# Performance work log

Hardware: AMD Instinct MI355X
Metric: run time of the kernel (lower is better)

The kernel has to match this reference:

```python
import jax, jax.numpy as jnp
import numpy as np

B, T, D_IN, D_H, D_CODE, N_CODES, D_OUT = 64, 512, 1024, 512, 256, 128, 100


def setup_inputs() -> dict:
    key = jax.random.key(0)
    ks = jax.random.split(key, 8)
    x = jax.random.normal(ks[0], (B, T, D_IN), dtype=jnp.float32)
    W1 = jax.random.normal(ks[1], (D_IN, D_H), dtype=jnp.float32) * (1.0 / np.sqrt(D_IN))
    b1 = jnp.zeros((D_H,), jnp.float32)
    W2 = jax.random.normal(ks[2], (D_H, D_CODE), dtype=jnp.float32) * (1.0 / np.sqrt(D_H))
    b2 = jnp.zeros((D_CODE,), jnp.float32)
    codebook = jax.random.normal(ks[3], (N_CODES, D_CODE), dtype=jnp.float32)
    Wd = jax.random.normal(ks[4], (D_CODE, D_OUT), dtype=jnp.float32) * (1.0 / np.sqrt(D_CODE))
    bd = jnp.zeros((D_OUT,), jnp.float32)
    return {"x": x, "W1": W1, "b1": b1, "W2": W2, "b2": b2,
            "codebook": codebook, "Wd": Wd, "bd": bd}


def reference(x, W1, b1, W2, b2, codebook, Wd, bd):
    Bb, Tt, _ = x.shape
    # Encoder (per-timestep loop in torch == one batched matmul)
    h = jax.nn.relu(jnp.einsum('btd,dh->bth', x, W1) + b1)
    encoded = jnp.einsum('bth,hc->btc', h, W2) + b2          # [B,T,256]
    flat = encoded.reshape(-1, D_CODE)                        # [B*T,256]
    # Squared euclidean distances (argmin identical to cdist argmin)
    d2 = (jnp.sum(flat * flat, axis=1, keepdims=True)
          - 2.0 * flat @ codebook.T
          + jnp.sum(codebook * codebook, axis=1))             # [B*T,128]
    token_indices = jnp.argmin(d2, axis=-1)                   # [B*T]
    quantized = codebook[token_indices].reshape(Bb, Tt, D_CODE)
    commitment_loss = jnp.mean((encoded - jax.lax.stop_gradient(quantized)) ** 2)
    codebook_loss = jnp.mean((quantized - jax.lax.stop_gradient(encoded)) ** 2)
    # decoded is computed in the torch model but never returned (dead code)
    pooled = encoded.mean(axis=1)
    decoded = pooled @ Wd + bd  # noqa: F841 (pruned by XLA, kept for fidelity)
    total_loss = commitment_loss + 0.25 * codebook_loss
    return (token_indices.reshape(Bb, Tt), commitment_loss, codebook_loss, total_loss)
```

## Files before the change

### kernel.cpp

```cpp
#include <hip/hip_runtime.h>
#include <cstddef>
#include <cstdint>

static constexpr int M_ROWS  = 32768;
static constexpr int D_INK   = 1024;
static constexpr int D_HID   = 512;
static constexpr int D_CODE_ = 256;
static constexpr int N_CODES_= 128;

static constexpr float TAU_GAP = 0.15f;

using f16x8 = __attribute__((ext_vector_type(8))) _Float16;
using f32x4 = __attribute__((ext_vector_type(4))) float;
using f32x2 = __attribute__((ext_vector_type(2))) float;

__device__ __forceinline__ float rdlane(float v, int kk) {
    return __uint_as_float(__builtin_amdgcn_readlane(__float_as_uint(v), kk));
}


__device__ __forceinline__ void dma16(const void* g, void* l) {
    __builtin_amdgcn_global_load_lds(
        (const __attribute__((address_space(1))) void*)g,
        (__attribute__((address_space(3))) void*)l, 16, 0, 0);
}

__device__ __forceinline__ void stage_panel(const _Float16* __restrict__ p,
                                            _Float16* dst, int w, int lane)
{
    #pragma unroll
    for (int ii = 0; ii < 2; ++ii) {
        const int I = 2 * w + ii;
        dma16(p + (size_t)I * 512 + lane * 8, dst + (size_t)I * 512);
    }
}

__device__ __forceinline__ void mfma_tile(const _Float16* sA, const _Float16* sB,
                                          int wm, int wn, int kq, int lm,
                                          f32x4 (&acc)[4][4])
{
    f16x8 a[4];
    #pragma unroll
    for (int fm = 0; fm < 4; ++fm)
        a[fm] = *(const f16x8*)(sA + (kq * 128 + wm * 64 + fm * 16 + lm) * 8);
    #pragma unroll
    for (int fn = 0; fn < 4; ++fn) {
        const f16x8 b = *(const f16x8*)(sB + (kq * 128 + wn * 64 + fn * 16 + lm) * 8);
        #pragma unroll
        for (int fm = 0; fm < 4; ++fm)
            acc[fm][fn] = __builtin_amdgcn_mfma_f32_16x16x32_f16(a[fm], b, acc[fm][fn], 0, 0, 0);
    }
}

__device__ __forceinline__ int xcd_swz(int bid, int nwg) {
    const int q = nwg >> 3;
    return (bid & 7) * q + (bid >> 3);
}

__global__ __launch_bounds__(256)
void prep_cb_kernel(const float* __restrict__ cb, _Float16* __restrict__ cbP,
                    float* __restrict__ cbT,
                    float* __restrict__ cbnorm, float* __restrict__ accum,
                    int* __restrict__ cnt)
{
    const int j = blockIdx.x;
    const int t = threadIdx.x;
    const float v = cb[j * D_CODE_ + t];
    const int ks = t >> 5, kq = (t >> 3) & 3, jj = t & 7;
    cbP[((size_t)ks * 512 + kq * 128 + j) * 8 + jj] = (_Float16)v;
    cbT[(size_t)t * N_CODES_ + j] = v;

    __shared__ float sr[256];
    sr[t] = v * v;
    __syncthreads();
    for (int s = 128; s >= 1; s >>= 1) {
        if (t < s) sr[t] += sr[t + s];
        __syncthreads();
    }
    if (t == 0) cbnorm[j] = sr[0];
    if (j == 0 && t < 2) accum[t] = 0.0f;
    if (j == 0 && t == 2) *cnt = 0;
}

__global__ __launch_bounds__(256)
void pack_w_kernel(const float* __restrict__ W, _Float16* __restrict__ WP,
                   int Kd, int Nd)
{
    const int ks = blockIdx.x, nt = blockIdx.y;
    const int t = threadIdx.x;
    _Float16* dst = WP + ((size_t)nt * (Kd >> 5) + ks) * 4096;
    #pragma unroll
    for (int half = 0; half < 2; ++half) {
        const int f = half * 256 + t;
        const int nc = f & 127, kq = f >> 7;
        f16x8 v;
        #pragma unroll
        for (int j = 0; j < 8; ++j)
            v[j] = (_Float16)W[(size_t)(ks * 32 + kq * 8 + j) * Nd + nt * 128 + nc];
        *(f16x8*)(dst + (size_t)f * 8) = v;
    }
}

__global__ __launch_bounds__(256)
void pack_x_kernel(const float* __restrict__ X, _Float16* __restrict__ XP)
{
    __shared__ _Float16 sh[128][136];
    const int t  = threadIdx.x;
    const int mt = blockIdx.x;
    const int kc = blockIdx.y;

    const float* src = X + (size_t)mt * 128 * D_INK + kc * 128;
    #pragma unroll
    for (int i = 0; i < 16; ++i) {
        const int idx = i * 256 + t;
        const int row = idx >> 5, c4 = idx & 31;
        const float4 v = *(const float4*)(src + (size_t)row * D_INK + c4 * 4);
        _Float16* d = &sh[row][c4 * 4];
        d[0] = (_Float16)v.x; d[1] = (_Float16)v.y;
        d[2] = (_Float16)v.z; d[3] = (_Float16)v.w;
    }
    __syncthreads();

    _Float16* dst = XP + ((size_t)mt * 32 + kc * 4) * 4096;
    #pragma unroll
    for (int s = 0; s < 4; ++s) {
        #pragma unroll
        for (int half = 0; half < 2; ++half) {
            const int f = half * 256 + t;
            const int rc = f & 127, kq = f >> 7;
            const f16x8 v = *(const f16x8*)(&sh[rc][s * 32 + kq * 8]);
            *(f16x8*)(dst + (size_t)s * 4096 + (size_t)f * 8) = v;
        }
    }
}

__global__ __launch_bounds__(256, 4)
void gemm1_kernel(const _Float16* __restrict__ AP, const _Float16* __restrict__ BP,
                  const float* __restrict__ bias, _Float16* __restrict__ CP)
{
    __shared__ _Float16 lds[2][2][4096];

    const int tid  = threadIdx.x;
    const int lane = tid & 63;
    const int w    = tid >> 6;
    const int wm = w >> 1, wn = w & 1;
    const int kq = lane >> 4, lm = lane & 15;

    const int swz = xcd_swz(blockIdx.x, (M_ROWS / 128) * (D_HID / 128));
    const int n0 = (swz & 3) * 128;
    const int m0 = (swz >> 2) * 128;

    const _Float16* Apan = AP + ((size_t)(m0 >> 7) * 32) * 4096;
    const _Float16* Bpan = BP + ((size_t)(n0 >> 7) * 32) * 4096;

    f32x4 acc[4][4] = {};

    stage_panel(Apan, &lds[0][0][0], w, lane);
    stage_panel(Bpan, &lds[0][1][0], w, lane);

    constexpr int NSTEP = D_INK / 32;
    for (int t = 0; t < NSTEP; ++t) {
        const int cur = t & 1, nxt = cur ^ 1;
        __syncthreads();
        if (t + 1 < NSTEP) {
            stage_panel(Apan + (size_t)(t + 1) * 4096, &lds[nxt][0][0], w, lane);
            stage_panel(Bpan + (size_t)(t + 1) * 4096, &lds[nxt][1][0], w, lane);
        }
        mfma_tile(&lds[cur][0][0], &lds[cur][1][0], wm, wn, kq, lm, acc);
    }

    #pragma unroll
    for (int fn = 0; fn < 4; ++fn) {
        const int col = n0 + wn * 64 + fn * 16 + lm;
        const float bv = bias[col];
        #pragma unroll
        for (int fm = 0; fm < 4; ++fm) {
            #pragma unroll
            for (int r = 0; r < 4; ++r) {
                const int row = m0 + wm * 64 + fm * 16 + kq * 4 + r;
                const float v = fmaxf(acc[fm][fn][r] + bv, 0.0f);
                CP[(((size_t)(row >> 7) * 16 + (col >> 5)) * 512
                    + (size_t)((col >> 3) & 3) * 128 + (row & 127)) * 8 + (col & 7)]
                    = (_Float16)v;
            }
        }
    }
}

__global__ __launch_bounds__(256, 4)
void gemm2_kernel(const _Float16* __restrict__ AP, const _Float16* __restrict__ BP,
                  const float* __restrict__ bias, _Float16* __restrict__ CP,
                  float* __restrict__ accum)
{
    __shared__ _Float16 lds[2][2][4096];

    const int tid  = threadIdx.x;
    const int lane = tid & 63;
    const int w    = tid >> 6;
    const int wm = w >> 1, wn = w & 1;
    const int kq = lane >> 4, lm = lane & 15;

    const int swz = xcd_swz(blockIdx.x, (M_ROWS / 128) * (D_CODE_ / 128));
    const int n0 = (swz & 1) * 128;
    const int m0 = (swz >> 1) * 128;

    const _Float16* Apan = AP + ((size_t)(m0 >> 7) * 16) * 4096;
    const _Float16* Bpan = BP + ((size_t)(n0 >> 7) * 16) * 4096;

    f32x4 acc[4][4] = {};

    stage_panel(Apan, &lds[0][0][0], w, lane);
    stage_panel(Bpan, &lds[0][1][0], w, lane);

    constexpr int NSTEP = D_HID / 32;
    for (int t = 0; t < NSTEP; ++t) {
        const int cur = t & 1, nxt = cur ^ 1;
        __syncthreads();
        if (t + 1 < NSTEP) {
            stage_panel(Apan + (size_t)(t + 1) * 4096, &lds[nxt][0][0], w, lane);
            stage_panel(Bpan + (size_t)(t + 1) * 4096, &lds[nxt][1][0], w, lane);
        }
        mfma_tile(&lds[cur][0][0], &lds[cur][1][0], wm, wn, kq, lm, acc);
    }

    float sumsq = 0.0f;
    #pragma unroll
    for (int fn = 0; fn < 4; ++fn) {
        const int col = n0 + wn * 64 + fn * 16 + lm;
        const float bv = bias[col];
        #pragma unroll
        for (int fm = 0; fm < 4; ++fm) {
            #pragma unroll
            for (int r = 0; r < 4; ++r) {
                const int row = m0 + wm * 64 + fm * 16 + kq * 4 + r;
                const float v = acc[fm][fn][r] + bv;
                sumsq = fmaf(v, v, sumsq);
                CP[(((size_t)(row >> 7) * 8 + (col >> 5)) * 512
                    + (size_t)((col >> 3) & 3) * 128 + (row & 127)) * 8 + (col & 7)]
                    = (_Float16)v;
            }
        }
    }
    #pragma unroll
    for (int mk = 1; mk <= 32; mk <<= 1) sumsq += __shfl_xor(sumsq, mk);
    if (lane == 0) atomicAdd(&accum[1], sumsq);
}

__global__ __launch_bounds__(256, 4)
void dist_kernel(const _Float16* __restrict__ AP, const _Float16* __restrict__ BP,
                 const float* __restrict__ cbn,
                 float* __restrict__ outIdx, float* __restrict__ accum,
                 int* __restrict__ cnt, int* __restrict__ list)
{
    __shared__ _Float16 lds[2][2][4096];

    const int tid  = threadIdx.x;
    const int lane = tid & 63;
    const int w    = tid >> 6;
    const int wm = w >> 1, wn = w & 1;
    const int kq = lane >> 4, lm = lane & 15;
    const int m0 = blockIdx.x * 128;

    float cbn_l[4];
    #pragma unroll
    for (int fn = 0; fn < 4; ++fn) cbn_l[fn] = cbn[wn * 64 + fn * 16 + lm];

    const _Float16* Apan = AP + ((size_t)(m0 >> 7) * 8) * 4096;

    f32x4 acc[4][4] = {};

    stage_panel(Apan, &lds[0][0][0], w, lane);
    stage_panel(BP,   &lds[0][1][0], w, lane);

    constexpr int NSTEP = D_CODE_ / 32;
    for (int t = 0; t < NSTEP; ++t) {
        const int cur = t & 1, nxt = cur ^ 1;
        __syncthreads();
        if (t + 1 < NSTEP) {
            stage_panel(Apan + (size_t)(t + 1) * 4096, &lds[nxt][0][0], w, lane);
            stage_panel(BP   + (size_t)(t + 1) * 4096, &lds[nxt][1][0], w, lane);
        }
        mfma_tile(&lds[cur][0][0], &lds[cur][1][0], wm, wn, kq, lm, acc);
    }

    __syncthreads();
    float* eb1 = (float*)&lds[0][0][0];
    float* eb2 = eb1 + 256;
    int*   eix = (int*)(eb2 + 256);

    #pragma unroll
    for (int fm = 0; fm < 4; ++fm) {
        #pragma unroll
        for (int r = 0; r < 4; ++r) {
            float b1v = 3.4e38f, b2v = 3.4e38f; int bi = 0;
            #pragma unroll
            for (int fn = 0; fn < 4; ++fn) {
                const float v = fmaf(-2.0f, acc[fm][fn][r], cbn_l[fn]);
                if (v < b1v) { b2v = b1v; b1v = v; bi = wn * 64 + fn * 16 + lm; }
                else if (v < b2v) b2v = v;
            }
            #pragma unroll
            for (int mk = 1; mk <= 8; mk <<= 1) {
                const float o1 = __shfl_xor(b1v, mk);
                const float o2 = __shfl_xor(b2v, mk);
                const int   oi = __shfl_xor(bi,  mk);
                if (o1 < b1v || (o1 == b1v && oi < bi)) { b2v = fminf(b1v, o2); b1v = o1; bi = oi; }
                else b2v = fminf(b2v, o1);
            }
            const int rl = wm * 64 + fm * 16 + kq * 4 + r;
            if (lm == 0) { eb1[wn * 128 + rl] = b1v; eb2[wn * 128 + rl] = b2v; eix[wn * 128 + rl] = bi; }
        }
    }
    __syncthreads();

    if (tid < 128) {
        const int rl = tid;
        const float a1 = eb1[rl], a2 = eb2[rl]; const int ai = eix[rl];
        const float o1 = eb1[128 + rl], o2 = eb2[128 + rl]; const int oi = eix[128 + rl];
        float B1, B2; int BI;
        if (o1 < a1 || (o1 == a1 && oi < ai)) { B1 = o1; BI = oi; B2 = fminf(a1, o2); }
        else                                  { B1 = a1; BI = ai; B2 = fminf(a2, o1); }
        outIdx[m0 + rl] = (float)BI;
        if (B2 - B1 < TAU_GAP) { const int p = atomicAdd(cnt, 1); list[p] = m0 + rl; }
        float s = B1;
        #pragma unroll
        for (int mk = 1; mk <= 32; mk <<= 1) s += __shfl_xor(s, mk);
        if (lane == 0) atomicAdd(&accum[0], s);
    }
}

__global__ __launch_bounds__(256)
void fixup_kernel(const float* __restrict__ x, const float* __restrict__ W1,
                  const float* __restrict__ b1, const float* __restrict__ W2,
                  const float* __restrict__ b2, const float* __restrict__ cbT,
                  const float* __restrict__ cbnorm,
                  const int* __restrict__ cnt, const int* __restrict__ list,
                  float* __restrict__ outIdx)
{
    __shared__ float xr[8][1024];
    __shared__ float hr[8][512];
    __shared__ float er[8][256];
    __shared__ float dv[8][128];
    __shared__ int   di[8][128];

    const int tid  = threadIdx.x;
    const int lane = tid & 63;
    const int n = *cnt;
    const int ngroups = (n + 7) >> 3;

    for (int g = blockIdx.x; g < ngroups; g += gridDim.x) {
        const int base = g * 8;
        const int nr = (n - base < 8) ? (n - base) : 8;
        __syncthreads();
        #pragma unroll
        for (int r = 0; r < 8; ++r) {
            if (r < nr) {
                const int row = list[base + r];
                *(float4*)&xr[r][tid * 4] =
                    *(const float4*)(x + (size_t)row * D_INK + tid * 4);
            }
        }
        __syncthreads();

        {
            const int c2 = tid * 2;
            f32x2 a01[8] = {};
            for (int k0 = 0; k0 < D_INK; k0 += 64) {
                float xreg[8];
                #pragma unroll
                for (int r = 0; r < 8; ++r) xreg[r] = xr[r][k0 + lane];
                #pragma unroll
                for (int kb = 0; kb < 64; kb += 8) {
                    f32x2 wv[8];
                    #pragma unroll
                    for (int p = 0; p < 8; ++p)
                        wv[p] = *(const f32x2*)&W1[(size_t)(k0 + kb + p) * D_HID + c2];
                    #pragma unroll
                    for (int p = 0; p < 8; ++p) {
                        const int kk = kb + p;
                        #pragma unroll
                        for (int r = 0; r < 8; ++r) {
                            const float xb = rdlane(xreg[r], kk);
                            a01[r] = __builtin_elementwise_fma((f32x2){xb, xb}, wv[p], a01[r]);
                        }
                    }
                }
            }
            #pragma unroll
            for (int r = 0; r < 8; ++r) {
                hr[r][c2]     = fmaxf(a01[r].x + b1[c2], 0.0f);
                hr[r][c2 + 1] = fmaxf(a01[r].y + b1[c2 + 1], 0.0f);
            }
        }
        __syncthreads();

        {
            const int cc = (tid & 127) * 2;
            const int half = tid >> 7;
            f32x2 a2[4] = {};
            for (int k0 = 0; k0 < D_HID; k0 += 64) {
                float hreg[4];
                #pragma unroll
                for (int q = 0; q < 4; ++q) hreg[q] = hr[half * 4 + q][k0 + lane];
                #pragma unroll
                for (int kb = 0; kb < 64; kb += 8) {
                    f32x2 wv[8];
                    #pragma unroll
                    for (int p = 0; p < 8; ++p)
                        wv[p] = *(const f32x2*)&W2[(size_t)(k0 + kb + p) * D_CODE_ + cc];
                    #pragma unroll
                    for (int p = 0; p < 8; ++p) {
                        const int kk = kb + p;
                        #pragma unroll
                        for (int q = 0; q < 4; ++q) {
                            const float hb = rdlane(hreg[q], kk);
                            a2[q] = __builtin_elementwise_fma((f32x2){hb, hb}, wv[p], a2[q]);
                        }
                    }
                }
            }
            #pragma unroll
            for (int q = 0; q < 4; ++q) {
                er[half * 4 + q][cc]     = a2[q].x + b2[cc];
                er[half * 4 + q][cc + 1] = a2[q].y + b2[cc + 1];
            }
        }
        __syncthreads();

        {
            const int j = tid & 127;
            const int half = tid >> 7;
            float e2[4], dt[4];
            #pragma unroll
            for (int q = 0; q < 4; ++q) { e2[q] = 0.0f; dt[q] = 0.0f; }
            for (int k0 = 0; k0 < D_CODE_; k0 += 64) {
                float ereg[4];
                #pragma unroll
                for (int q = 0; q < 4; ++q) ereg[q] = er[half * 4 + q][k0 + lane];
                #pragma unroll
                for (int kb = 0; kb < 64; kb += 8) {
                    float cv[8];
                    #pragma unroll
                    for (int p = 0; p < 8; ++p)
                        cv[p] = cbT[(size_t)(k0 + kb + p) * N_CODES_ + j];
                    #pragma unroll
                    for (int p = 0; p < 8; ++p) {
                        const int kk = kb + p;
                        #pragma unroll
                        for (int q = 0; q < 4; ++q) {
                            const float ev = rdlane(ereg[q], kk);
                            e2[q] = fmaf(ev, ev, e2[q]);
                            dt[q] = fmaf(ev, cv[p], dt[q]);
                        }
                    }
                }
            }
            #pragma unroll
            for (int q = 0; q < 4; ++q) {
                dv[half * 4 + q][j] = (e2[q] - 2.0f * dt[q]) + cbnorm[j];
                di[half * 4 + q][j] = j;
            }
        }
        __syncthreads();

        #pragma unroll
        for (int pass = 0; pass < 4; ++pass) {
            const int r = pass * 2 + (tid >> 7);
            const int i = tid & 127;
            for (int st = 64; st >= 1; st >>= 1) {
                if (i < st) {
                    const float a = dv[r][i], b = dv[r][i + st];
                    const int  ib = di[r][i + st];
                    if (b < a || (b == a && ib < di[r][i])) { dv[r][i] = b; di[r][i] = ib; }
                }
                __syncthreads();
            }
        }
        if (tid < nr) outIdx[list[base + tid]] = (float)di[tid][0];
    }
}

__global__ void finalize_kernel(const float* __restrict__ accum, float* __restrict__ out)
{
    const float inv = 1.0f / (32768.0f * 256.0f);
    const float loss = (accum[0] + accum[1]) * inv;
    out[32768] = loss;
    out[32769] = loss;
    out[32770] = 1.25f * loss;
}

extern "C" void kernel_launch(void* const* d_in, const int* in_sizes, int n_in,
                              void* d_out, int out_size, void* d_ws, size_t ws_size,
                              hipStream_t stream)
{
    (void)in_sizes; (void)n_in; (void)out_size; (void)ws_size;

    const float* x  = (const float*)d_in[0];
    const float* W1 = (const float*)d_in[1];
    const float* b1 = (const float*)d_in[2];
    const float* W2 = (const float*)d_in[3];
    const float* b2 = (const float*)d_in[4];
    const float* cb = (const float*)d_in[5];
    float* out = (float*)d_out;

    char* ws = (char*)d_ws;
    _Float16* W1P  = (_Float16*)(ws + 0);
    _Float16* W2P  = (_Float16*)(ws + 1048576);
    _Float16* cbP  = (_Float16*)(ws + 1310720);
    float*    cbn  = (float*   )(ws + 1376256);
    float*    accum= (float*   )(ws + 1376768);
    int*      cnt  = (int*     )(ws + 1376832);
    int*      list = (int*     )(ws + 1376896);
    float*    cbT  = (float*   )(ws + 1507968);
    _Float16* xP   = (_Float16*)(ws + (size_t)(2u<<20));
    _Float16* encP = (_Float16*)(ws + (size_t)(2u<<20));
    _Float16* hP   = (_Float16*)(ws + (size_t)(2u<<20) + 67108864);

    prep_cb_kernel<<<N_CODES_, 256, 0, stream>>>(cb, cbP, cbT, cbn, accum, cnt);
    pack_w_kernel<<<dim3(D_INK / 32, D_HID / 128), 256, 0, stream>>>(W1, W1P, D_INK, D_HID);
    pack_w_kernel<<<dim3(D_HID / 32, D_CODE_ / 128), 256, 0, stream>>>(W2, W2P, D_HID, D_CODE_);
    pack_x_kernel<<<dim3(M_ROWS / 128, D_INK / 128), 256, 0, stream>>>(x, xP);

    gemm1_kernel<<<(M_ROWS / 128) * (D_HID / 128), 256, 0, stream>>>(xP, W1P, b1, hP);
    gemm2_kernel<<<(M_ROWS / 128) * (D_CODE_ / 128), 256, 0, stream>>>(hP, W2P, b2, encP, accum);
    dist_kernel<<<M_ROWS / 128, 256, 0, stream>>>(encP, cbP, cbn, out, accum, cnt, list);
    fixup_kernel<<<512, 256, 0, stream>>>(x, W1, b1, W2, b2, cbT, cbn, cnt, list, out);
    finalize_kernel<<<1, 1, 0, stream>>>(accum, out);
}
```

Measured before the change: 246.5 us.

## Recheck ambiguous rows with split-fp16 MFMA GEMMs before scalar fp32 fixup

```diff
diff --git a/kernel.cpp b/kernel.cpp
--- a/kernel.cpp
+++ b/kernel.cpp
@@ -9,6 +9,7 @@
 static constexpr int N_CODES_= 128;
 
 static constexpr float TAU_GAP = 0.15f;
+static constexpr float TAU2_GAP = 0.005f;
 
 using f16x8 = __attribute__((ext_vector_type(8))) _Float16;
 using f32x4 = __attribute__((ext_vector_type(4))) float;
@@ -52,6 +53,32 @@
     }
 }
 
+__device__ __forceinline__ void mfma_tile3(const _Float16* sAh, const _Float16* sAl,
+                                           const _Float16* sBh, const _Float16* sBl,
+                                           int wm, int wn, int kq, int lm,
+                                           f32x4 (&acc)[4][4])
+{
+    f16x8 ah[4], al[4];
+    #pragma unroll
+    for (int fm = 0; fm < 4; ++fm) {
+        const int fA = kq * 128 + wm * 64 + fm * 16 + lm;
+        ah[fm] = *(const f16x8*)(sAh + fA * 8);
+        al[fm] = *(const f16x8*)(sAl + fA * 8);
+    }
+    #pragma unroll
+    for (int fn = 0; fn < 4; ++fn) {
+        const int fB = kq * 128 + wn * 64 + fn * 16 + lm;
+        const f16x8 bh = *(const f16x8*)(sBh + fB * 8);
+        const f16x8 bl = *(const f16x8*)(sBl + fB * 8);
+        #pragma unroll
+        for (int fm = 0; fm < 4; ++fm) {
+            acc[fm][fn] = __builtin_amdgcn_mfma_f32_16x16x32_f16(ah[fm], bh, acc[fm][fn], 0, 0, 0);
+            acc[fm][fn] = __builtin_amdgcn_mfma_f32_16x16x32_f16(al[fm], bh, acc[fm][fn], 0, 0, 0);
+            acc[fm][fn] = __builtin_amdgcn_mfma_f32_16x16x32_f16(ah[fm], bl, acc[fm][fn], 0, 0, 0);
+        }
+    }
+}
+
 __device__ __forceinline__ int xcd_swz(int bid, int nwg) {
     const int q = nwg >> 3;
     return (bid & 7) * q + (bid >> 3);
@@ -59,15 +86,17 @@
 
 __global__ __launch_bounds__(256)
 void prep_cb_kernel(const float* __restrict__ cb, _Float16* __restrict__ cbP,
-                    float* __restrict__ cbT,
+                    _Float16* __restrict__ cbPl, float* __restrict__ cbT,
                     float* __restrict__ cbnorm, float* __restrict__ accum,
-                    int* __restrict__ cnt)
+                    int* __restrict__ cnt, int* __restrict__ cnt2)
 {
     const int j = blockIdx.x;
     const int t = threadIdx.x;
     const float v = cb[j * D_CODE_ + t];
     const int ks = t >> 5, kq = (t >> 3) & 3, jj = t & 7;
-    cbP[((size_t)ks * 512 + kq * 128 + j) * 8 + jj] = (_Float16)v;
+    const _Float16 hi = (_Float16)v;
+    cbP [((size_t)ks * 512 + kq * 128 + j) * 8 + jj] = hi;
+    cbPl[((size_t)ks * 512 + kq * 128 + j) * 8 + jj] = (_Float16)(v - (float)hi);
     cbT[(size_t)t * N_CODES_ + j] = v;
 
     __shared__ float sr[256];
@@ -80,24 +109,30 @@
     if (t == 0) cbnorm[j] = sr[0];
     if (j == 0 && t < 2) accum[t] = 0.0f;
     if (j == 0 && t == 2) *cnt = 0;
+    if (j == 0 && t == 3) *cnt2 = 0;
 }
 
 __global__ __launch_bounds__(256)
-void pack_w_kernel(const float* __restrict__ W, _Float16* __restrict__ WP,
-                   int Kd, int Nd)
+void pack_w_kernel(const float* __restrict__ W, _Float16* __restrict__ WPh,
+                   _Float16* __restrict__ WPl, int Kd, int Nd)
 {
     const int ks = blockIdx.x, nt = blockIdx.y;
     const int t = threadIdx.x;
-    _Float16* dst = WP + ((size_t)nt * (Kd >> 5) + ks) * 4096;
+    const size_t pbase = ((size_t)nt * (Kd >> 5) + ks) * 4096;
     #pragma unroll
     for (int half = 0; half < 2; ++half) {
         const int f = half * 256 + t;
         const int nc = f & 127, kq = f >> 7;
-        f16x8 v;
-        #pragma unroll
-        for (int j = 0; j < 8; ++j)
-            v[j] = (_Float16)W[(size_t)(ks * 32 + kq * 8 + j) * Nd + nt * 128 + nc];
-        *(f16x8*)(dst + (size_t)f * 8) = v;
+        f16x8 vh, vl;
+        #pragma unroll
+        for (int j = 0; j < 8; ++j) {
+            const float w = W[(size_t)(ks * 32 + kq * 8 + j) * Nd + nt * 128 + nc];
+            const _Float16 hi = (_Float16)w;
+            vh[j] = hi;
+            vl[j] = (_Float16)(w - (float)hi);
+        }
+        *(f16x8*)(WPh + pbase + (size_t)f * 8) = vh;
+        *(f16x8*)(WPl + pbase + (size_t)f * 8) = vl;
     }
 }
 
@@ -321,7 +356,10 @@
         if (o1 < a1 || (o1 == a1 && oi < ai)) { B1 = o1; BI = oi; B2 = fminf(a1, o2); }
         else                                  { B1 = a1; BI = ai; B2 = fminf(a2, o1); }
         outIdx[m0 + rl] = (float)BI;
-        if (B2 - B1 < TAU_GAP) { const int p = atomicAdd(cnt, 1); list[p] = m0 + rl; }
+        if (B2 - B1 < TAU_GAP) {
+            const int p = atomicAdd(cnt, 1);
+            if (p < 32768) list[p] = m0 + rl;
+        }
         float s = B1;
         #pragma unroll
         for (int mk = 1; mk <= 32; mk <<= 1) s += __shfl_xor(s, mk);
@@ -330,12 +368,287 @@
 }
 
 __global__ __launch_bounds__(256)
-void fixup_kernel(const float* __restrict__ x, const float* __restrict__ W1,
-                  const float* __restrict__ b1, const float* __restrict__ W2,
-                  const float* __restrict__ b2, const float* __restrict__ cbT,
-                  const float* __restrict__ cbnorm,
-                  const int* __restrict__ cnt, const int* __restrict__ list,
-                  float* __restrict__ outIdx)
+void gather_pack_fix_kernel(const float* __restrict__ X,
+                            const int* __restrict__ list, const int* __restrict__ cnt,
+                            _Float16* __restrict__ XH, _Float16* __restrict__ XL)
+{
+    __shared__ _Float16 shh[64][136];
+    __shared__ _Float16 shl[64][136];
+    const int n = *cnt;
+    if (n == 0) return;
+    const int ntp = (n + 127) >> 7;
+    const int ht = blockIdx.x;
+    if (ht >= ntp * 2) return;
+    const int kc = blockIdx.y;
+    const int t = threadIdx.x;
+
+    #pragma unroll
+    for (int i = 0; i < 8; ++i) {
+        const int idx = i * 256 + t;
+        const int rl = idx >> 5;
+        const int c4 = idx & 31;
+        const int slot = ht * 64 + rl;
+        const int srcrow = list[slot < n ? slot : n - 1];
+        const float4 v = *(const float4*)(X + (size_t)srcrow * D_INK + kc * 128 + c4 * 4);
+        _Float16* dh = &shh[rl][c4 * 4];
+        _Float16* dl = &shl[rl][c4 * 4];
+        const float vv[4] = {v.x, v.y, v.z, v.w};
+        #pragma unroll
+        for (int q = 0; q < 4; ++q) {
+            const _Float16 hi = (_Float16)vv[q];
+            dh[q] = hi;
+            dl[q] = (_Float16)(vv[q] - (float)hi);
+        }
+    }
+    __syncthreads();
+
+    const int rl = t & 63, kq = t >> 6;
+    const int rc = (ht & 1) * 64 + rl;
+    const size_t pb = ((size_t)(ht >> 1) * 32 + kc * 4) * 4096;
+    #pragma unroll
+    for (int s = 0; s < 4; ++s) {
+        const size_t off = pb + (size_t)s * 4096 + (size_t)(kq * 128 + rc) * 8;
+        *(f16x8*)(XH + off) = *(const f16x8*)(&shh[rl][s * 32 + kq * 8]);
+        *(f16x8*)(XL + off) = *(const f16x8*)(&shl[rl][s * 32 + kq * 8]);
+    }
+}
+
+__global__ __launch_bounds__(256, 2)
+void gemm1_fix_kernel(const _Float16* __restrict__ AH, const _Float16* __restrict__ AL,
+                      const _Float16* __restrict__ BH, const _Float16* __restrict__ BL,
+                      const float* __restrict__ bias,
+                      _Float16* __restrict__ CH, _Float16* __restrict__ CL,
+                      const int* __restrict__ cnt)
+{
+    __shared__ _Float16 lds[2][4][4096];
+    const int n = *cnt;
+    const int ntp = (n + 127) >> 7;
+    if ((int)blockIdx.x >= ntp) return;
+
+    const int tid  = threadIdx.x;
+    const int lane = tid & 63;
+    const int w    = tid >> 6;
+    const int wm = w >> 1, wn = w & 1;
+    const int kq = lane >> 4, lm = lane & 15;
+    const int m0 = blockIdx.x * 128;
+    const int n0 = blockIdx.y * 128;
+
+    const _Float16* Ah = AH + ((size_t)blockIdx.x * 32) * 4096;
+    const _Float16* Al = AL + ((size_t)blockIdx.x * 32) * 4096;
+    const _Float16* Bh = BH + ((size_t)blockIdx.y * 32) * 4096;
+    const _Float16* Bl = BL + ((size_t)blockIdx.y * 32) * 4096;
+
+    f32x4 acc[4][4] = {};
+
+    stage_panel(Ah, &lds[0][0][0], w, lane);
+    stage_panel(Al, &lds[0][1][0], w, lane);
+    stage_panel(Bh, &lds[0][2][0], w, lane);
+    stage_panel(Bl, &lds[0][3][0], w, lane);
+
+    constexpr int NSTEP = D_INK / 32;
+    for (int t = 0; t < NSTEP; ++t) {
+        const int cur = t & 1, nxt = cur ^ 1;
+        __syncthreads();
+        if (t + 1 < NSTEP) {
+            stage_panel(Ah + (size_t)(t + 1) * 4096, &lds[nxt][0][0], w, lane);
+            stage_panel(Al + (size_t)(t + 1) * 4096, &lds[nxt][1][0], w, lane);
+            stage_panel(Bh + (size_t)(t + 1) * 4096, &lds[nxt][2][0], w, lane);
+            stage_panel(Bl + (size_t)(t + 1) * 4096, &lds[nxt][3][0], w, lane);
+        }
+        mfma_tile3(&lds[cur][0][0], &lds[cur][1][0], &lds[cur][2][0], &lds[cur][3][0],
+                   wm, wn, kq, lm, acc);
+    }
+
+    #pragma unroll
+    for (int fn = 0; fn < 4; ++fn) {
+        const int col = n0 + wn * 64 + fn * 16 + lm;
+        const float bv = bias[col];
+        #pragma unroll
+        for (int fm = 0; fm < 4; ++fm) {
+            #pragma unroll
+            for (int r = 0; r < 4; ++r) {
+                const int row = m0 + wm * 64 + fm * 16 + kq * 4 + r;
+                const float v = fmaxf(acc[fm][fn][r] + bv, 0.0f);
+                const _Float16 hi = (_Float16)v;
+                const size_t idx = (((size_t)(row >> 7) * 16 + (col >> 5)) * 512
+                    + (size_t)((col >> 3) & 3) * 128 + (row & 127)) * 8 + (col & 7);
+                CH[idx] = hi;
+                CL[idx] = (_Float16)(v - (float)hi);
+            }
+        }
+    }
+}
+
+__global__ __launch_bounds__(256, 2)
+void gemm2_fix_kernel(const _Float16* __restrict__ AH, const _Float16* __restrict__ AL,
+                      const _Float16* __restrict__ BH, const _Float16* __restrict__ BL,
+                      const float* __restrict__ bias,
+                      _Float16* __restrict__ CH, _Float16* __restrict__ CL,
+                      const int* __restrict__ cnt)
+{
+    __shared__ _Float16 lds[2][4][4096];
+    const int n = *cnt;
+    const int ntp = (n + 127) >> 7;
+    if ((int)blockIdx.x >= ntp) return;
+
+    const int tid  = threadIdx.x;
+    const int lane = tid & 63;
+    const int w    = tid >> 6;
+    const int wm = w >> 1, wn = w & 1;
+    const int kq = lane >> 4, lm = lane & 15;
+    const int m0 = blockIdx.x * 128;
+    const int n0 = blockIdx.y * 128;
+
+    const _Float16* Ah = AH + ((size_t)blockIdx.x * 16) * 4096;
+    const _Float16* Al = AL + ((size_t)blockIdx.x * 16) * 4096;
+    const _Float16* Bh = BH + ((size_t)blockIdx.y * 16) * 4096;
+    const _Float16* Bl = BL + ((size_t)blockIdx.y * 16) * 4096;
+
+    f32x4 acc[4][4] = {};
+
+    stage_panel(Ah, &lds[0][0][0], w, lane);
+    stage_panel(Al, &lds[0][1][0], w, lane);
+    stage_panel(Bh, &lds[0][2][0], w, lane);
+    stage_panel(Bl, &lds[0][3][0], w, lane);
+
+    constexpr int NSTEP = D_HID / 32;
+    for (int t = 0; t < NSTEP; ++t) {
+        const int cur = t & 1, nxt = cur ^ 1;
+        __syncthreads();
+        if (t + 1 < NSTEP) {
+            stage_panel(Ah + (size_t)(t + 1) * 4096, &lds[nxt][0][0], w, lane);
+            stage_panel(Al + (size_t)(t + 1) * 4096, &lds[nxt][1][0], w, lane);
+            stage_panel(Bh + (size_t)(t + 1) * 4096, &lds[nxt][2][0], w, lane);
+            stage_panel(Bl + (size_t)(t + 1) * 4096, &lds[nxt][3][0], w, lane);
+        }
+        mfma_tile3(&lds[cur][0][0], &lds[cur][1][0], &lds[cur][2][0], &lds[cur][3][0],
+                   wm, wn, kq, lm, acc);
+    }
+
+    #pragma unroll
+    for (int fn = 0; fn < 4; ++fn) {
+        const int col = n0 + wn * 64 + fn * 16 + lm;
+        const float bv = bias[col];
+        #pragma unroll
+        for (int fm = 0; fm < 4; ++fm) {
+            #pragma unroll
+            for (int r = 0; r < 4; ++r) {
+                const int row = m0 + wm * 64 + fm * 16 + kq * 4 + r;
+                const float v = acc[fm][fn][r] + bv;
+                const _Float16 hi = (_Float16)v;
+                const size_t idx = (((size_t)(row >> 7) * 8 + (col >> 5)) * 512
+                    + (size_t)((col >> 3) & 3) * 128 + (row & 127)) * 8 + (col & 7);
+                CH[idx] = hi;
+                CL[idx] = (_Float16)(v - (float)hi);
+            }
+        }
+    }
+}
+
+__global__ __launch_bounds__(256, 2)
+void dist_fix_kernel(const _Float16* __restrict__ AH, const _Float16* __restrict__ AL,
+                     const _Float16* __restrict__ BH, const _Float16* __restrict__ BL,
+                     const float* __restrict__ cbn,
+                     const int* __restrict__ list, const int* __restrict__ cnt,
+                     float* __restrict__ outIdx,
+                     int* __restrict__ cnt2, int* __restrict__ list2)
+{
+    __shared__ _Float16 lds[2][4][4096];
+    const int n = *cnt;
+    const int ntp = (n + 127) >> 7;
+    if ((int)blockIdx.x >= ntp) return;
+
+    const int tid  = threadIdx.x;
+    const int lane = tid & 63;
+    const int w    = tid >> 6;
+    const int wm = w >> 1, wn = w & 1;
+    const int kq = lane >> 4, lm = lane & 15;
+    const int m0 = blockIdx.x * 128;
+
+    float cbn_l[4];
+    #pragma unroll
+    for (int fn = 0; fn < 4; ++fn) cbn_l[fn] = cbn[wn * 64 + fn * 16 + lm];
+
+    const _Float16* Ah = AH + ((size_t)blockIdx.x * 8) * 4096;
+    const _Float16* Al = AL + ((size_t)blockIdx.x * 8) * 4096;
+
+    f32x4 acc[4][4] = {};
+
+    stage_panel(Ah, &lds[0][0][0], w, lane);
+    stage_panel(Al, &lds[0][1][0], w, lane);
+    stage_panel(BH, &lds[0][2][0], w, lane);
+    stage_panel(BL, &lds[0][3][0], w, lane);
+
+    constexpr int NSTEP = D_CODE_ / 32;
+    for (int t = 0; t < NSTEP; ++t) {
+        const int cur = t & 1, nxt = cur ^ 1;
+        __syncthreads();
+        if (t + 1 < NSTEP) {
+            stage_panel(Ah + (size_t)(t + 1) * 4096, &lds[nxt][0][0], w, lane);
+            stage_panel(Al + (size_t)(t + 1) * 4096, &lds[nxt][1][0], w, lane);
+            stage_panel(BH + (size_t)(t + 1) * 4096, &lds[nxt][2][0], w, lane);
+            stage_panel(BL + (size_t)(t + 1) * 4096, &lds[nxt][3][0], w, lane);
+        }
+        mfma_tile3(&lds[cur][0][0], &lds[cur][1][0], &lds[cur][2][0], &lds[cur][3][0],
+                   wm, wn, kq, lm, acc);
+    }
+
+    __syncthreads();
+    float* eb1 = (float*)&lds[0][0][0];
+    float* eb2 = eb1 + 256;
+    int*   eix = (int*)(eb2 + 256);
+
+    #pragma unroll
+    for (int fm = 0; fm < 4; ++fm) {
+        #pragma unroll
+        for (int r = 0; r < 4; ++r) {
+            float b1v = 3.4e38f, b2v = 3.4e38f; int bi = 0;
+            #pragma unroll
+            for (int fn = 0; fn < 4; ++fn) {
+                const float v = fmaf(-2.0f, acc[fm][fn][r], cbn_l[fn]);
+                if (v < b1v) { b2v = b1v; b1v = v; bi = wn * 64 + fn * 16 + lm; }
+                else if (v < b2v) b2v = v;
+            }
+            #pragma unroll
+            for (int mk = 1; mk <= 8; mk <<= 1) {
+                const float o1 = __shfl_xor(b1v, mk);
+                const float o2 = __shfl_xor(b2v, mk);
+                const int   oi = __shfl_xor(bi,  mk);
+                if (o1 < b1v || (o1 == b1v && oi < bi)) { b2v = fminf(b1v, o2); b1v = o1; bi = oi; }
+                else b2v = fminf(b2v, o1);
+            }
+            const int rl = wm * 64 + fm * 16 + kq * 4 + r;
+            if (lm == 0) { eb1[wn * 128 + rl] = b1v; eb2[wn * 128 + rl] = b2v; eix[wn * 128 + rl] = bi; }
+        }
+    }
+    __syncthreads();
+
+    if (tid < 128) {
+        const int slot = m0 + tid;
+        if (slot < n) {
+            const int rl = tid;
+            const float a1 = eb1[rl], a2 = eb2[rl]; const int ai = eix[rl];
+            const float o1 = eb1[128 + rl], o2 = eb2[128 + rl]; const int oi = eix[128 + rl];
+            float B1, B2; int BI;
+            if (o1 < a1 || (o1 == a1 && oi < ai)) { B1 = o1; BI = oi; B2 = fminf(a1, o2); }
+            else                                  { B1 = a1; BI = ai; B2 = fminf(a2, o1); }
+            const int row = list[slot];
+            outIdx[row] = (float)BI;
+            if (B2 - B1 < TAU2_GAP) {
+                const int p = atomicAdd(cnt2, 1);
+                if (p < 8192) list2[p] = row;
+            }
+        }
+    }
+}
+
+__global__ __launch_bounds__(256)
+void fixup2_kernel(const float* __restrict__ x, const float* __restrict__ W1,
+                   const float* __restrict__ b1, const float* __restrict__ W2,
+                   const float* __restrict__ b2, const float* __restrict__ cbT,
+                   const float* __restrict__ cbnorm,
+                   const int* __restrict__ cnt2, const int* __restrict__ list2,
+                   float* __restrict__ outIdx)
 {
     __shared__ float xr[8][1024];
     __shared__ float hr[8][512];
@@ -345,7 +658,7 @@
 
     const int tid  = threadIdx.x;
     const int lane = tid & 63;
-    const int n = *cnt;
+    const int n = *cnt2;
     const int ngroups = (n + 7) >> 3;
 
     for (int g = blockIdx.x; g < ngroups; g += gridDim.x) {
@@ -355,7 +668,7 @@
         #pragma unroll
         for (int r = 0; r < 8; ++r) {
             if (r < nr) {
-                const int row = list[base + r];
+                const int row = list2[base + r];
                 *(float4*)&xr[r][tid * 4] =
                     *(const float4*)(x + (size_t)row * D_INK + tid * 4);
             }
@@ -476,7 +789,7 @@
                 __syncthreads();
             }
         }
-        if (tid < nr) outIdx[list[base + tid]] = (float)di[tid][0];
+        if (tid < nr) outIdx[list2[base + tid]] = (float)di[tid][0];
     }
 }
 
@@ -504,26 +817,44 @@
     float* out = (float*)d_out;
 
     char* ws = (char*)d_ws;
-    _Float16* W1P  = (_Float16*)(ws + 0);
-    _Float16* W2P  = (_Float16*)(ws + 1048576);
-    _Float16* cbP  = (_Float16*)(ws + 1310720);
-    float*    cbn  = (float*   )(ws + 1376256);
-    float*    accum= (float*   )(ws + 1376768);
-    int*      cnt  = (int*     )(ws + 1376832);
-    int*      list = (int*     )(ws + 1376896);
-    float*    cbT  = (float*   )(ws + 1507968);
-    _Float16* xP   = (_Float16*)(ws + (size_t)(2u<<20));
-    _Float16* encP = (_Float16*)(ws + (size_t)(2u<<20));
-    _Float16* hP   = (_Float16*)(ws + (size_t)(2u<<20) + 67108864);
-
-    prep_cb_kernel<<<N_CODES_, 256, 0, stream>>>(cb, cbP, cbT, cbn, accum, cnt);
-    pack_w_kernel<<<dim3(D_INK / 32, D_HID / 128), 256, 0, stream>>>(W1, W1P, D_INK, D_HID);
-    pack_w_kernel<<<dim3(D_HID / 32, D_CODE_ / 128), 256, 0, stream>>>(W2, W2P, D_HID, D_CODE_);
+    _Float16* W1P   = (_Float16*)(ws + 0);
+    _Float16* W1Pl  = (_Float16*)(ws + (1u<<20));
+    _Float16* W2P   = (_Float16*)(ws + (2u<<20));
+    _Float16* W2Pl  = (_Float16*)(ws + (2u<<20) + 262144);
+    _Float16* cbP   = (_Float16*)(ws + (2u<<20) + 524288);
+    _Float16* cbPl  = (_Float16*)(ws + (2u<<20) + 589824);
+    float*    cbT   = (float*   )(ws + (2u<<20) + 655360);
+    float*    cbn   = (float*   )(ws + (2u<<20) + 786432);
+    float*    accum = (float*   )(ws + (2u<<20) + 786944);
+    int*      cnt   = (int*     )(ws + (2u<<20) + 787008);
+    int*      cnt2  = (int*     )(ws + (2u<<20) + 787072);
+    int*      list  = (int*     )(ws + (2u<<20) + 787136);
+    int*      list2 = (int*     )(ws + (2u<<20) + 918208);
+
+    _Float16* xP    = (_Float16*)(ws + (size_t)(4u<<20));
+    _Float16* encP  = (_Float16*)(ws + (size_t)(4u<<20));
+    _Float16* xfPh  = (_Float16*)(ws + (size_t)(4u<<20) + 16777216);
+    _Float16* xfPl  = (_Float16*)(ws + (size_t)(4u<<20) + 33554432);
+    _Float16* hP    = (_Float16*)(ws + (size_t)(68u<<20));
+    _Float16* hfPh  = (_Float16*)(ws + (size_t)(68u<<20));
+    _Float16* hfPl  = (_Float16*)(ws + (size_t)(68u<<20) + 8388608);
+    _Float16* encfPh= (_Float16*)(ws + (size_t)(68u<<20) + 16777216);
+    _Float16* encfPl= (_Float16*)(ws + (size_t)(68u<<20) + 20971520);
+
+    prep_cb_kernel<<<N_CODES_, 256, 0, stream>>>(cb, cbP, cbPl, cbT, cbn, accum, cnt, cnt2);
+    pack_w_kernel<<<dim3(D_INK / 32, D_HID / 128), 256, 0, stream>>>(W1, W1P, W1Pl, D_INK, D_HID);
+    pack_w_kernel<<<dim3(D_HID / 32, D_CODE_ / 128), 256, 0, stream>>>(W2, W2P, W2Pl, D_HID, D_CODE_);
     pack_x_kernel<<<dim3(M_ROWS / 128, D_INK / 128), 256, 0, stream>>>(x, xP);
 
     gemm1_kernel<<<(M_ROWS / 128) * (D_HID / 128), 256, 0, stream>>>(xP, W1P, b1, hP);
     gemm2_kernel<<<(M_ROWS / 128) * (D_CODE_ / 128), 256, 0, stream>>>(hP, W2P, b2, encP, accum);
     dist_kernel<<<M_ROWS / 128, 256, 0, stream>>>(encP, cbP, cbn, out, accum, cnt, list);
-    fixup_kernel<<<512, 256, 0, stream>>>(x, W1, b1, W2, b2, cbT, cbn, cnt, list, out);
+
+    gather_pack_fix_kernel<<<dim3(128, 8), 256, 0, stream>>>(x, list, cnt, xfPh, xfPl);
+    gemm1_fix_kernel<<<dim3(64, 4), 256, 0, stream>>>(xfPh, xfPl, W1P, W1Pl, b1, hfPh, hfPl, cnt);
+    gemm2_fix_kernel<<<dim3(64, 2), 256, 0, stream>>>(hfPh, hfPl, W2P, W2Pl, b2, encfPh, encfPl, cnt);
+    dist_fix_kernel<<<64, 256, 0, stream>>>(encfPh, encfPl, cbP, cbPl, cbn,
+                                            list, cnt, out, cnt2, list2);
+    fixup2_kernel<<<64, 256, 0, stream>>>(x, W1, b1, W2, b2, cbT, cbn, cnt2, list2, out);
     finalize_kernel<<<1, 1, 0, stream>>>(accum, out);
 }
```

Measured after the change: 307.9 us. +24.9%, slower.
